# Performance work log

Measured on AMD Instinct MI355X. Metric: run time of the kernel, lower is better.

The kernel has to match this reference:

```python
import jax, jax.numpy as jnp
import numpy as np
from functools import partial

LEAK = 1.0 / 3.0   # scn default leakiness 0.333
EPS = 1e-4         # scn BatchNormalization default eps


def linkey(c, S):
    return (c[..., 0] * S + c[..., 1]) * S + c[..., 2]


def sub_offsets(K):
    r = K // 2
    g = np.stack(np.meshgrid(*([np.arange(-r, r + 1)] * 3), indexing='ij'), -1).reshape(-1, 3)
    return jnp.asarray(g, jnp.int32)


def down_offsets(s):
    g = np.stack(np.meshgrid(*([np.arange(s)] * 3), indexing='ij'), -1).reshape(-1, 3)
    return jnp.asarray(g, jnp.int32)


@partial(jax.checkpoint, static_argnums=(4, 5))
def sparse_conv(out_coords, in_coords, in_feats, W, S_in, stride, offsets):
    """Rulebook gather-GEMM-scatter via sorted-key binary search.
    out_coords [M,3], in_coords [N,3] sorted by linearized key, in_feats [N,Cin],
    W [K3,Cin,Cout]. Submanifold: stride=1, centered offsets, out_coords==in_coords.
    Strided scn.Convolution: offsets 0..stride-1, out sites = unique(in//stride)."""
    in_keys = linkey(in_coords, S_in)  # sorted [N]
    Nin = in_keys.shape[0]

    def body(acc, kw):
        off, Wk = kw
        child = out_coords * stride + off                       # [M,3]
        valid = jnp.all((child >= 0) & (child < S_in), axis=-1)
        nkey = linkey(child, S_in)
        idx = jnp.searchsorted(in_keys, nkey)
        idxc = jnp.clip(idx, 0, Nin - 1)
        found = valid & (in_keys[idxc] == nkey)
        g = jnp.where(found[:, None], in_feats[idxc], 0.0)      # gather, zero for inactive
        return acc + g @ Wk, None

    acc0 = jnp.zeros((out_coords.shape[0], W.shape[-1]), in_feats.dtype)
    acc, _ = jax.lax.scan(body, acc0, (offsets, W))
    return acc


def bn_lrelu(x, g, b):
    m = x.mean(0)
    v = x.var(0)
    y = (x - m) * (g / jnp.sqrt(v + EPS)) + b
    return jnp.where(y > 0, y, LEAK * y)


def lrelu(x):
    return jnp.where(x > 0, x, LEAK * x)


def forward_core(floats, c0, c1, c2, c3, c4):
    (feats0, W_init, Wd1, gd1, bd1, W11a, g11, b11, W11b,
     W12a, g12, b12, W12b, Wd2, gd2, bd2,
     W21a, g21, b21, W21b, W22a, g22, b22, W22b,
     Wd3, gd3, bd3, Wd4, gd4, bd4, W2, b2, W3, b3) = floats
    o3 = sub_offsets(3)
    x = sparse_conv(c0, c0, feats0, W_init, 512, 1, sub_offsets(7))                 # [N0,64] @512
    x = bn_lrelu(sparse_conv(c1, c0, x, Wd1, 512, 2, down_offsets(2)), gd1, bd1)    # [N1,64] @256
    res = x
    h = bn_lrelu(sparse_conv(c1, c1, x, W11a, 256, 1, o3), g11, b11)
    x = lrelu(sparse_conv(c1, c1, h, W11b, 256, 1, o3) + res)
    res = x
    h = bn_lrelu(sparse_conv(c1, c1, x, W12a, 256, 1, o3), g12, b12)
    x = lrelu(sparse_conv(c1, c1, h, W12b, 256, 1, o3) + res)
    x = bn_lrelu(sparse_conv(c2, c1, x, Wd2, 256, 2, down_offsets(2)), gd2, bd2)    # [N2,128] @128
    res = x
    h = bn_lrelu(sparse_conv(c2, c2, x, W21a, 128, 1, o3), g21, b21)
    x = lrelu(sparse_conv(c2, c2, h, W21b, 128, 1, o3) + res)
    res = x
    h = bn_lrelu(sparse_conv(c2, c2, x, W22a, 128, 1, o3), g22, b22)
    x = lrelu(sparse_conv(c2, c2, h, W22b, 128, 1, o3) + res)
    x = bn_lrelu(sparse_conv(c3, c2, x, Wd3, 128, 4, down_offsets(4)), gd3, bd3)    # [N3,64] @32
    x = bn_lrelu(sparse_conv(c4, c3, x, Wd4, 32, 4, down_offsets(4)), gd4, bd4)     # [N4,2]  @8
    # SparseToDense -> dense [2,8,8,8], then torch .view(-1, 2*8*8*8) (channel-major)
    k4 = linkey(c4, 8)
    dense = jnp.zeros((8 * 8 * 8, 2), x.dtype).at[k4].set(x)    # [512,2]
    flat = dense.T.reshape(1, -1)                               # [1,1024]
    v = jax.nn.elu(flat @ W2 + b2)
    return jax.nn.sigmoid(v @ W3 + b3)                          # [1,1]


def _decode(k, S):
    a = k // (S * S)
    r = k % (S * S)
    return np.stack([a, r // S, r % S], -1).astype(np.int32)


def setup_inputs() -> dict:
    rng = np.random.default_rng(0)
    N0 = 50000
    k0 = np.unique(rng.integers(0, 512 ** 3, size=N0 + 20000))[:N0]
    c0 = _decode(k0, 512)
    c1 = _decode(np.unique((c0[:, 0].astype(np.int64) // 2 * 256 + c0[:, 1] // 2) * 256 + c0[:, 2] // 2), 256)
    c2 = _decode(np.unique((c1[:, 0].astype(np.int64) // 2 * 128 + c1[:, 1] // 2) * 128 + c1[:, 2] // 2), 128)
    c3 = _decode(np.unique((c2[:, 0].astype(np.int64) // 4 * 32 + c2[:, 1] // 4) * 32 + c2[:, 2] // 4), 32)
    c4 = _decode(np.unique((c3[:, 0].astype(np.int64) // 4 * 8 + c3[:, 1] // 4) * 8 + c3[:, 2] // 4), 8)
    key = jax.random.key(0)
    ks = jax.random.split(key, 20)

    def w(i, shape, fan):
        return jax.random.normal(ks[i], shape, jnp.float32) / np.float32(np.sqrt(fan))

    return dict(
        feats0=jax.random.normal(ks[0], (N0, 1), jnp.float32),
        W_init=w(1, (343, 1, 64), 343.0),
        Wd1=w(2, (8, 64, 64), 8 * 64), gd1=jnp.ones(64), bd1=jnp.zeros(64),
        W11a=w(3, (27, 64, 64), 27 * 64), g11=jnp.ones(64), b11=jnp.zeros(64),
        W11b=w(4, (27, 64, 64), 27 * 64),
        W12a=w(5, (27, 64, 64), 27 * 64), g12=jnp.ones(64), b12=jnp.zeros(64),
        W12b=w(6, (27, 64, 64), 27 * 64),
        Wd2=w(7, (8, 64, 128), 8 * 64), gd2=jnp.ones(128), bd2=jnp.zeros(128),
        W21a=w(8, (27, 128, 128), 27 * 128), g21=jnp.ones(128), b21=jnp.zeros(128),
        W21b=w(9, (27, 128, 128), 27 * 128),
        W22a=w(10, (27, 128, 128), 27 * 128), g22=jnp.ones(128), b22=jnp.zeros(128),
        W22b=w(11, (27, 128, 128), 27 * 128),
        Wd3=w(12, (64, 128, 64), 64 * 128), gd3=jnp.ones(64), bd3=jnp.zeros(64),
        Wd4=w(13, (64, 64, 2), 64 * 64), gd4=jnp.ones(2), bd4=jnp.zeros(2),
        W2=w(14, (1024, 2), 1024.0), b2=jnp.zeros(2),
        W3=w(15, (2, 1), 2.0), b3=jnp.zeros(1),
        coords0=jnp.asarray(c0), coords1=jnp.asarray(c1), coords2=jnp.asarray(c2),
        coords3=jnp.asarray(c3), coords4=jnp.asarray(c4),
    )


def reference(feats0, W_init, Wd1, gd1, bd1, W11a, g11, b11, W11b, W12a, g12, b12, W12b,
              Wd2, gd2, bd2, W21a, g21, b21, W21b, W22a, g22, b22, W22b,
              Wd3, gd3, bd3, Wd4, gd4, bd4, W2, b2, W3, b3,
              coords0, coords1, coords2, coords3, coords4):
    floats = (feats0, W_init, Wd1, gd1, bd1, W11a, g11, b11, W11b, W12a, g12, b12, W12b,
              Wd2, gd2, bd2, W21a, g21, b21, W21b, W22a, g22, b22, W22b,
              Wd3, gd3, bd3, Wd4, gd4, bd4, W2, b2, W3, b3)
    return forward_core(floats, coords0, coords1, coords2, coords3, coords4)
```

## Files before the change

### kernel.cpp

```cpp
#include <hip/hip_runtime.h>

#define LEAKF (1.0f/3.0f)
#define BN_EPS 1e-4f

__device__ __forceinline__ unsigned hmix(int key) {
    unsigned h = (unsigned)key * 2654435761u;
    h ^= h >> 15;
    return h;
}

__device__ __forceinline__ int hlookup(const int* __restrict__ hk,
                                       const int* __restrict__ hv,
                                       int mask, int key) {
    unsigned h = hmix(key) & (unsigned)mask;
    while (true) {
        int k = hk[h];
        if (k == key) return hv[h];
        if (k == -1) return -1;
        h = (h + 1) & (unsigned)mask;
    }
}

__global__ void build_hash(const int* __restrict__ coords, int N, int S,
                           int* __restrict__ hk, int* __restrict__ hv, int mask) {
    int i = blockIdx.x * blockDim.x + threadIdx.x;
    if (i >= N) return;
    int key = (coords[3 * i] * S + coords[3 * i + 1]) * S + coords[3 * i + 2];
    unsigned h = hmix(key) & (unsigned)mask;
    while (true) {
        int old = atomicCAS(&hk[h], -1, key);
        if (old == -1 || old == key) { hv[h] = i; break; }
        h = (h + 1) & (unsigned)mask;
    }
}

__global__ void build_bitmap(const int* __restrict__ coords, int N,
                             unsigned* __restrict__ bm) {
    int i = blockIdx.x * blockDim.x + threadIdx.x;
    if (i >= N) return;
    int key = (coords[3 * i] * 512 + coords[3 * i + 1]) * 512 + coords[3 * i + 2];
    atomicOr(&bm[key >> 5], 1u << (key & 31));
}

__device__ __forceinline__ float bnl(float v, float s, float h) {
    v = v * s + h;
    return v > 0.f ? v : v * LEAKF;
}

__global__ __launch_bounds__(256) void rb_sub(
    int N, const int* __restrict__ coords,
    const int* __restrict__ hk, const int* __restrict__ hv, int mask,
    int S, int2* __restrict__ pairs, int* __restrict__ counts, int cap) {
    __shared__ int lcnt[27];
    __shared__ int lbase[27];
    int tid = threadIdx.x;
    if (tid < 27) lcnt[tid] = 0;
    __syncthreads();
    int t = blockIdx.x * 256 + tid;
    int k = -1, m = -1, idx = -1, rank = 0;
    if (t < N * 26) {
        m = t / 26;
        int kt = t - m * 26;
        k = kt < 13 ? kt : kt + 1;
        int a = k / 9, b = (k / 3) % 3, c = k % 3;
        int x = coords[3 * m] + a - 1;
        int y = coords[3 * m + 1] + b - 1;
        int z = coords[3 * m + 2] + c - 1;
        if ((unsigned)x < (unsigned)S && (unsigned)y < (unsigned)S &&
            (unsigned)z < (unsigned)S) {
            idx = hlookup(hk, hv, mask, (x * S + y) * S + z);
            if (idx >= 0) rank = atomicAdd(&lcnt[k], 1);
        }
    }
    __syncthreads();
    if (tid < 27 && lcnt[tid] > 0) lbase[tid] = atomicAdd(&counts[tid], lcnt[tid]);
    __syncthreads();
    if (idx >= 0) {
        int p = lbase[k] + rank;
        if (p < cap) pairs[(size_t)k * cap + p] = make_int2(m, idx);
    }
}

__global__ __launch_bounds__(256) void rb_down(
    int Nin, const int* __restrict__ cin,
    const int* __restrict__ hk, const int* __restrict__ hv, int mask,
    int Sout, int s, int2* __restrict__ pairs, int* __restrict__ counts, int cap) {
    __shared__ int lcnt[64];
    __shared__ int lbase[64];
    int tid = threadIdx.x;
    int K3 = s * s * s;
    if (tid < K3) lcnt[tid] = 0;
    __syncthreads();
    int i = blockIdx.x * 256 + tid;
    int k = -1, m = -1, rank = 0;
    if (i < Nin) {
        int x = cin[3 * i], y = cin[3 * i + 1], z = cin[3 * i + 2];
        k = ((x % s) * s + (y % s)) * s + (z % s);
        int key = ((x / s) * Sout + (y / s)) * Sout + (z / s);
        m = hlookup(hk, hv, mask, key);
        rank = atomicAdd(&lcnt[k], 1);
    }
    __syncthreads();
    if (tid < K3 && lcnt[tid] > 0) lbase[tid] = atomicAdd(&counts[tid], lcnt[tid]);
    __syncthreads();
    if (i < Nin) {
        int p = lbase[k] + rank;
        if (p < cap) pairs[(size_t)k * cap + p] = make_int2(m, i);
    }
}

__global__ __launch_bounds__(256) void init_probe(
    int total, const int* __restrict__ c0, const unsigned* __restrict__ bm,
    const int* __restrict__ hk, const int* __restrict__ hv, int mask,
    int2* __restrict__ pairs, int* __restrict__ pcount, int cap) {
    __shared__ int lcnt, lbase;
    int tid = threadIdx.x;
    if (tid == 0) lcnt = 0;
    __syncthreads();
    int t = blockIdx.x * 256 + tid;
    unsigned bits = 0;
    int m = -1, kmin = 0, z = 0, dx = 0, dy = 0, rank = 0;
    if (t < total) {
        m = t / 49;
        int od = t - m * 49;
        dx = od / 7 - 3;
        dy = od - (od / 7) * 7 - 3;
        int x = c0[3 * m] + dx;
        int y = c0[3 * m + 1] + dy;
        z = c0[3 * m + 2];
        if ((unsigned)x < 512u && (unsigned)y < 512u) {
            int zmin = z - 3 < 0 ? 0 : z - 3;
            int zmax = z + 3 > 511 ? 511 : z + 3;
            kmin = (x * 512 + y) * 512 + zmin;
            int wi = kmin >> 5, sh = kmin & 31, nb = zmax - zmin + 1;
            unsigned long long w =
                ((unsigned long long)bm[wi + 1] << 32) | (unsigned long long)bm[wi];
            bits = (unsigned)((w >> sh) & ((1u << nb) - 1u));
            if (dx == 0 && dy == 0) bits &= ~(1u << (z - zmin));
            if (bits) rank = atomicAdd(&lcnt, __popc(bits));
        }
    }
    __syncthreads();
    if (tid == 0 && lcnt > 0) lbase = atomicAdd(pcount, lcnt);
    __syncthreads();
    while (bits) {
        int b = __ffs(bits) - 1;
        bits &= bits - 1;
        int nkey = kmin + b;
        int idx = hlookup(hk, hv, mask, nkey);
        int dz = (kmin & 511) + b - z;
        int k = (dx + 3) * 49 + (dy + 3) * 7 + (dz + 3);
        int p = lbase + rank++;
        if (p < cap) pairs[p] = make_int2(m, idx | (k << 17));
    }
}

__global__ __launch_bounds__(256) void init_center(
    int N0, const float* __restrict__ f0, const float* __restrict__ W,
    float* __restrict__ out) {
    int t = blockIdx.x * 256 + threadIdx.x;
    if (t >= N0 * 64) return;
    int m = t >> 6, co = t & 63;
    out[t] = f0[m] * W[171 * 64 + co];
}

__global__ __launch_bounds__(256) void init_apply(
    const int2* __restrict__ pairs, const int* __restrict__ pcount, int cap,
    const float* __restrict__ f0, const float* __restrict__ W,
    float* __restrict__ out) {
    int P = min(*pcount, cap);
    int t = blockIdx.x * 256 + threadIdx.x;
    if (t >= P * 64) return;
    int p = t >> 6, co = t & 63;
    int2 pr = pairs[p];
    int idx = pr.y & 0x1FFFF, k = pr.y >> 17;
    atomicAdd(&out[(size_t)pr.x * 64 + co], f0[idx] * W[k * 64 + co]);
}

template <int C, int TS, bool BNF>
__global__ __launch_bounds__(256) void center_gemm(
    int N, const float* __restrict__ inF, const float* __restrict__ Wc,
    float* __restrict__ out, const float* __restrict__ scp,
    const float* __restrict__ shp) {
    constexpr int C4 = C / 4;
    constexpr int SP = TS / 8;
    __shared__ float sW[C * 64];
    __shared__ float4 sRow[TS * C4];
    int tid = threadIdx.x;
    int t0 = blockIdx.x * TS;
    int co0 = blockIdx.y << 6;
    for (int e = tid; e < C * 16; e += 256) {
        int ci = e >> 4, c4 = e & 15;
        ((float4*)sW)[e] = *(const float4*)(Wc + (size_t)ci * C + co0 + c4 * 4);
    }
    for (int e = tid; e < TS * C4; e += 256) {
        int p = e / C4, c4 = e - p * C4;
        float4 v = make_float4(0.f, 0.f, 0.f, 0.f);
        if (t0 + p < N) {
            v = ((const float4*)inF)[(size_t)(t0 + p) * C4 + c4];
            if (BNF) {
                float4 s4 = ((const float4*)scp)[c4];
                float4 h4 = ((const float4*)shp)[c4];
                v.x = bnl(v.x, s4.x, h4.x);
                v.y = bnl(v.y, s4.y, h4.y);
                v.z = bnl(v.z, s4.z, h4.z);
                v.w = bnl(v.w, s4.w, h4.w);
            }
        }
        sRow[e] = v;
    }
    __syncthreads();
    int co = tid & 31, sg = tid >> 5;
    float accA[SP], accB[SP];
#pragma unroll
    for (int j = 0; j < SP; j++) { accA[j] = 0.f; accB[j] = 0.f; }
    for (int c4 = 0; c4 < C4; c4++) {
        float a0 = sW[(c4 * 4 + 0) * 64 + co];
        float a1 = sW[(c4 * 4 + 1) * 64 + co];
        float a2 = sW[(c4 * 4 + 2) * 64 + co];
        float a3 = sW[(c4 * 4 + 3) * 64 + co];
        float b0 = sW[(c4 * 4 + 0) * 64 + co + 32];
        float b1 = sW[(c4 * 4 + 1) * 64 + co + 32];
        float b2 = sW[(c4 * 4 + 2) * 64 + co + 32];
        float b3 = sW[(c4 * 4 + 3) * 64 + co + 32];
#pragma unroll
        for (int j = 0; j < SP; j++) {
            float4 r = sRow[(sg * SP + j) * C4 + c4];
            accA[j] += r.x * a0 + r.y * a1 + r.z * a2 + r.w * a3;
            accB[j] += r.x * b0 + r.y * b1 + r.z * b2 + r.w * b3;
        }
    }
#pragma unroll
    for (int j = 0; j < SP; j++) {
        int p = sg * SP + j;
        if (t0 + p < N) {
            out[(size_t)(t0 + p) * C + co0 + co] = accA[j];
            out[(size_t)(t0 + p) * C + co0 + co + 32] = accB[j];
        }
    }
}

template <int CIN, int P, bool BNF>
__global__ __launch_bounds__(256) void pair_gemm(
    const float* __restrict__ inF, const float* __restrict__ W, float* __restrict__ out,
    const int2* __restrict__ pairs, const int* __restrict__ counts,
    int cap, int chunksPerK, int COUT,
    const float* __restrict__ scp, const float* __restrict__ shp) {
    constexpr int C4 = CIN / 4;
    constexpr int SP = P / 8;
    __shared__ float sW[CIN * 64];
    __shared__ float4 sRow[P * C4];
    __shared__ int sM[P];
    __shared__ int sIdx[P];
    int k = blockIdx.x / chunksPerK;
    int chunk = blockIdx.x - k * chunksPerK;
    int cnt = min(counts[k], cap);
    int base = chunk * P;
    if (base >= cnt) return;
    int Pact = min(P, cnt - base);
    int tid = threadIdx.x;
    if (tid < P) {
        if (tid < Pact) {
            int2 pr = pairs[(size_t)k * cap + base + tid];
            sM[tid] = pr.x;
            sIdx[tid] = pr.y;
        } else {
            sM[tid] = -1;
            sIdx[tid] = 0;
        }
    }
    __syncthreads();
    int co0 = blockIdx.y << 6;
    const float* gW = W + (size_t)k * CIN * COUT + co0;
    for (int e = tid; e < CIN * 16; e += 256) {
        int ci = e >> 4, c4 = e & 15;
        ((float4*)sW)[e] = *(const float4*)(gW + (size_t)ci * COUT + c4 * 4);
    }
    for (int e = tid; e < P * C4; e += 256) {
        int p = e / C4, c4 = e - p * C4;
        float4 v = make_float4(0.f, 0.f, 0.f, 0.f);
        if (p < Pact) {
            v = ((const float4*)inF)[(size_t)sIdx[p] * C4 + c4];
            if (BNF) {
                float4 s4 = ((const float4*)scp)[c4];
                float4 h4 = ((const float4*)shp)[c4];
                v.x = bnl(v.x, s4.x, h4.x);
                v.y = bnl(v.y, s4.y, h4.y);
                v.z = bnl(v.z, s4.z, h4.z);
                v.w = bnl(v.w, s4.w, h4.w);
            }
        }
        sRow[e] = v;
    }
    __syncthreads();
    int co = tid & 31, sg = tid >> 5;
    float accA[SP], accB[SP];
#pragma unroll
    for (int j = 0; j < SP; j++) { accA[j] = 0.f; accB[j] = 0.f; }
    for (int c4 = 0; c4 < C4; c4++) {
        float a0 = sW[(c4 * 4 + 0) * 64 + co];
        float a1 = sW[(c4 * 4 + 1) * 64 + co];
        float a2 = sW[(c4 * 4 + 2) * 64 + co];
        float a3 = sW[(c4 * 4 + 3) * 64 + co];
        float b0 = sW[(c4 * 4 + 0) * 64 + co + 32];
        float b1 = sW[(c4 * 4 + 1) * 64 + co + 32];
        float b2 = sW[(c4 * 4 + 2) * 64 + co + 32];
        float b3 = sW[(c4 * 4 + 3) * 64 + co + 32];
#pragma unroll
        for (int j = 0; j < SP; j++) {
            float4 r = sRow[(sg * SP + j) * C4 + c4];
            accA[j] += r.x * a0 + r.y * a1 + r.z * a2 + r.w * a3;
            accB[j] += r.x * b0 + r.y * b1 + r.z * b2 + r.w * b3;
        }
    }
#pragma unroll
    for (int j = 0; j < SP; j++) {
        int p = sg * SP + j;
        if (p < Pact) {
            atomicAdd(&out[(size_t)sM[p] * COUT + co0 + co], accA[j]);
            atomicAdd(&out[(size_t)sM[p] * COUT + co0 + co + 32], accB[j]);
        }
    }
}

__global__ __launch_bounds__(64) void convd4_kernel(
    int M, const int* __restrict__ oc, const float* __restrict__ x3,
    const float* __restrict__ W, float* __restrict__ out4,
    const int* __restrict__ hk, const int* __restrict__ hv, int mask,
    const float* __restrict__ scp, const float* __restrict__ shp) {
    __shared__ int sIdx[64];
    __shared__ int sK[64];
    __shared__ int sCount;
    int m = blockIdx.x, tid = threadIdx.x;
    int cx = oc[3 * m], cy = oc[3 * m + 1], cz = oc[3 * m + 2];
    if (tid == 0) sCount = 0;
    __syncthreads();
    {
        int k = tid;
        int a = k >> 4, b = (k >> 2) & 3, c = k & 3;
        int x = cx * 4 + a, y = cy * 4 + b, z = cz * 4 + c;
        int key = (x * 32 + y) * 32 + z;
        int idx = hlookup(hk, hv, mask, key);
        if (idx >= 0) { int p = atomicAdd(&sCount, 1); sIdx[p] = idx; sK[p] = k; }
    }
    __syncthreads();
    int cnt = sCount;
    float s = scp[tid], h = shp[tid];
    float a0 = 0.f, a1 = 0.f;
    for (int j = 0; j < cnt; j++) {
        int idx = sIdx[j], k = sK[j];
        float f = bnl(x3[(size_t)idx * 64 + tid], s, h);
        const float* wk = W + ((size_t)k * 64 + tid) * 2;
        a0 += f * wk[0];
        a1 += f * wk[1];
    }
    for (int o = 32; o > 0; o >>= 1) {
        a0 += __shfl_down(a0, o);
        a1 += __shfl_down(a1, o);
    }
    if (tid == 0) { out4[2 * m] = a0; out4[2 * m + 1] = a1; }
}

__global__ __launch_bounds__(256) void bn_reduce_fin(
    const float4* __restrict__ X4, int total4, int B4, int C, int Cmask, float invN,
    const float* __restrict__ g, const float* __restrict__ b,
    float* __restrict__ sums, int* __restrict__ done,
    float* __restrict__ sc, float* __restrict__ sh) {
    __shared__ float sS[128];
    __shared__ float sQ[128];
    __shared__ int isLast;
    int tid = threadIdx.x;
    if (tid < C) { sS[tid] = 0.f; sQ[tid] = 0.f; }
    __syncthreads();
    int base4 = blockIdx.x * B4;
    int end4 = min(base4 + B4, total4);
    float s0 = 0.f, s1 = 0.f, s2 = 0.f, s3 = 0.f;
    float q0 = 0.f, q1 = 0.f, q2 = 0.f, q3 = 0.f;
    for (int e4 = base4 + tid; e4 < end4; e4 += 256) {
        float4 v = X4[e4];
        s0 += v.x; q0 += v.x * v.x;
        s1 += v.y; q1 += v.y * v.y;
        s2 += v.z; q2 += v.z * v.z;
        s3 += v.w; q3 += v.w * v.w;
    }
    int c0 = (4 * (base4 + tid)) & Cmask;
    atomicAdd(&sS[c0], s0);           atomicAdd(&sQ[c0], q0);
    atomicAdd(&sS[(c0 + 1) & Cmask], s1); atomicAdd(&sQ[(c0 + 1) & Cmask], q1);
    atomicAdd(&sS[(c0 + 2) & Cmask], s2); atomicAdd(&sQ[(c0 + 2) & Cmask], q2);
    atomicAdd(&sS[(c0 + 3) & Cmask], s3); atomicAdd(&sQ[(c0 + 3) & Cmask], q3);
    __syncthreads();
    if (tid < C) {
        atomicAdd(&sums[tid], sS[tid]);
        atomicAdd(&sums[128 + tid], sQ[tid]);
    }
    __syncthreads();
    if (tid == 0) {
        __threadfence();
        int t = atomicAdd(done, 1);
        isLast = (t == (int)gridDim.x - 1);
    }
    __syncthreads();
    if (isLast) {
        if (tid < C) {
            float v1 = atomicAdd(&sums[tid], 0.0f);
            float v2 = atomicAdd(&sums[128 + tid], 0.0f);
            float mean = v1 * invN;
            float var = v2 * invN - mean * mean;
            float s = g[tid] / sqrtf(var + BN_EPS);
            sc[tid] = s;
            sh[tid] = b[tid] - mean * s;
            sums[tid] = 0.f;
            sums[128 + tid] = 0.f;
        }
        if (tid == 0) *done = 0;
    }
}

__global__ __launch_bounds__(256) void add_lrelu(const float4* __restrict__ A,
                                                 const float4* __restrict__ R,
                                                 float4* __restrict__ Y, int total4) {
    int e = blockIdx.x * 256 + threadIdx.x;
    if (e >= total4) return;
    float4 a = A[e], r = R[e], v;
    v.x = a.x + r.x; v.y = a.y + r.y; v.z = a.z + r.z; v.w = a.w + r.w;
    v.x = v.x > 0.f ? v.x : v.x * LEAKF;
    v.y = v.y > 0.f ? v.y : v.y * LEAKF;
    v.z = v.z > 0.f ? v.z : v.z * LEAKF;
    v.w = v.w > 0.f ? v.w : v.w * LEAKF;
    Y[e] = v;
}

__global__ __launch_bounds__(256) void add_lrelu_bn(const float4* __restrict__ A,
                                                    const float4* __restrict__ X,
                                                    float4* __restrict__ Y, int total4,
                                                    int C4mask,
                                                    const float* __restrict__ scp,
                                                    const float* __restrict__ shp) {
    int e = blockIdx.x * 256 + threadIdx.x;
    if (e >= total4) return;
    int c4 = e & C4mask;
    float4 s4 = ((const float4*)scp)[c4];
    float4 h4 = ((const float4*)shp)[c4];
    float4 a = A[e], x = X[e], v;
    v.x = a.x + bnl(x.x, s4.x, h4.x);
    v.y = a.y + bnl(x.y, s4.y, h4.y);
    v.z = a.z + bnl(x.z, s4.z, h4.z);
    v.w = a.w + bnl(x.w, s4.w, h4.w);
    v.x = v.x > 0.f ? v.x : v.x * LEAKF;
    v.y = v.y > 0.f ? v.y : v.y * LEAKF;
    v.z = v.z > 0.f ? v.z : v.z * LEAKF;
    v.w = v.w > 0.f ? v.w : v.w * LEAKF;
    Y[e] = v;
}

__global__ __launch_bounds__(256) void bn_scatter(int M, const int* __restrict__ c4,
                                                  const float* __restrict__ x4,
                                                  const float* __restrict__ sc,
                                                  const float* __restrict__ sh,
                                                  float* __restrict__ dense) {
    int i = blockIdx.x * 256 + threadIdx.x;
    if (i >= 2 * M) return;
    int m = i >> 1, co = i & 1;
    float v = x4[i] * sc[co] + sh[co];
    v = v > 0.f ? v : v * LEAKF;
    int key = (c4[3 * m] * 8 + c4[3 * m + 1]) * 8 + c4[3 * m + 2];
    dense[key * 2 + co] = v;
}

__global__ __launch_bounds__(256) void head_kernel(const float* __restrict__ dense,
                                                   const float* __restrict__ W2,
                                                   const float* __restrict__ b2,
                                                   const float* __restrict__ W3,
                                                   const float* __restrict__ b3,
                                                   float* __restrict__ out) {
    __shared__ float r0[256];
    __shared__ float r1[256];
    int tid = threadIdx.x;
    float a0 = 0.f, a1 = 0.f;
    for (int j = tid; j < 1024; j += 256) {
        int co = j >> 9, k = j & 511;
        float f = dense[k * 2 + co];
        a0 += f * W2[2 * j];
        a1 += f * W2[2 * j + 1];
    }
    r0[tid] = a0;
    r1[tid] = a1;
    __syncthreads();
    for (int s = 128; s > 0; s >>= 1) {
        if (tid < s) { r0[tid] += r0[tid + s]; r1[tid] += r1[tid + s]; }
        __syncthreads();
    }
    if (tid == 0) {
        float v0 = r0[0] + b2[0];
        float v1 = r1[0] + b2[1];
        v0 = v0 > 0.f ? v0 : expm1f(v0);
        v1 = v1 > 0.f ? v1 : expm1f(v1);
        float z = v0 * W3[0] + v1 * W3[1] + b3[0];
        out[0] = 1.f / (1.f + expf(-z));
    }
}

extern "C" void kernel_launch(void* const* d_in, const int* in_sizes, int n_in,
                              void* d_out, int out_size, void* d_ws, size_t ws_size,
                              hipStream_t stream) {
    const float* F0    = (const float*)d_in[0];
    const float* Winit = (const float*)d_in[1];
    const float* Wd1   = (const float*)d_in[2];
    const float* gd1   = (const float*)d_in[3];
    const float* bd1   = (const float*)d_in[4];
    const float* W11a  = (const float*)d_in[5];
    const float* g11   = (const float*)d_in[6];
    const float* b11   = (const float*)d_in[7];
    const float* W11b  = (const float*)d_in[8];
    const float* W12a  = (const float*)d_in[9];
    const float* g12   = (const float*)d_in[10];
    const float* b12   = (const float*)d_in[11];
    const float* W12b  = (const float*)d_in[12];
    const float* Wd2   = (const float*)d_in[13];
    const float* gd2   = (const float*)d_in[14];
    const float* bd2   = (const float*)d_in[15];
    const float* W21a  = (const float*)d_in[16];
    const float* g21   = (const float*)d_in[17];
    const float* b21   = (const float*)d_in[18];
    const float* W21b  = (const float*)d_in[19];
    const float* W22a  = (const float*)d_in[20];
    const float* g22   = (const float*)d_in[21];
    const float* b22   = (const float*)d_in[22];
    const float* W22b  = (const float*)d_in[23];
    const float* Wd3   = (const float*)d_in[24];
    const float* gd3   = (const float*)d_in[25];
    const float* bd3   = (const float*)d_in[26];
    const float* Wd4   = (const float*)d_in[27];
    const float* gd4   = (const float*)d_in[28];
    const float* bd4   = (const float*)d_in[29];
    const float* W2    = (const float*)d_in[30];
    const float* b2    = (const float*)d_in[31];
    const float* W3    = (const float*)d_in[32];
    const float* b3    = (const float*)d_in[33];
    const int* c0 = (const int*)d_in[34];
    const int* c1 = (const int*)d_in[35];
    const int* c2 = (const int*)d_in[36];
    const int* c3 = (const int*)d_in[37];
    const int* c4 = (const int*)d_in[38];
    int N0 = in_sizes[34] / 3, N1 = in_sizes[35] / 3, N2 = in_sizes[36] / 3;
    int N3 = in_sizes[37] / 3, N4 = in_sizes[38] / 3;

    char* base = (char*)d_ws;
    size_t off = 0;
    auto alloc = [&](size_t bytes) -> void* {
        void* p = base + off;
        off = (off + bytes + 255) & ~(size_t)255;
        return p;
    };
    const int CAP0 = 262144, CAP = 131072, CAP3 = 65536;
    size_t hs_off = off;
    int* hk0 = (int*)alloc((size_t)CAP0 * 4);
    int* hv0 = (int*)alloc((size_t)CAP0 * 4);
    int* hk1 = (int*)alloc((size_t)CAP * 4);
    int* hv1 = (int*)alloc((size_t)CAP * 4);
    int* hk2 = (int*)alloc((size_t)CAP * 4);
    int* hv2 = (int*)alloc((size_t)CAP * 4);
    int* hk3 = (int*)alloc((size_t)CAP3 * 4);
    int* hv3 = (int*)alloc((size_t)CAP3 * 4);
    size_t he_off = off;
    size_t zs_off = off;
    float* sums = (float*)alloc(256 * 4);
    float* scb = (float*)alloc(8 * 128 * 4);
    float* shb = (float*)alloc(8 * 128 * 4);
    float* dense = (float*)alloc(1024 * 4);
    float* x4 = (float*)alloc(1032 * 4);
    int* counts = (int*)alloc(136 * 4);
    size_t ze_off = off;
    int* cntS1 = counts, *cntS2 = counts + 27, *cntD1 = counts + 54, *cntD2 = counts + 62,
       * cntD3 = counts + 70;
    int* done = counts + 134;
    int* pcount = counts + 135;
    const int CAP_S1 = 1024, CAP_S2 = 4096, CAP_D1 = 8192, CAP_D2 = 8192, CAP_D3 = 1024;
    const int CAPP = 16384;
    int2* pairs0 = (int2*)alloc((size_t)CAPP * 8);
    int2* rbS1 = (int2*)alloc((size_t)27 * CAP_S1 * 8);
    int2* rbS2 = (int2*)alloc((size_t)27 * CAP_S2 * 8);
    int2* rbD1 = (int2*)alloc((size_t)8 * CAP_D1 * 8);
    int2* rbD2 = (int2*)alloc((size_t)8 * CAP_D2 * 8);
    int2* rbD3 = (int2*)alloc((size_t)64 * CAP_D3 * 8);
    size_t relems = (size_t)N0 * 64;
    if ((size_t)N2 * 128 > relems) relems = (size_t)N2 * 128;
    float* R1 = (float*)alloc(relems * 4);
    float* R2 = (float*)alloc(relems * 4);
    float* R3 = (float*)alloc(relems * 4);
    unsigned* bitmap = (unsigned*)R1;

    hipMemsetAsync(base + hs_off, 0xFF, he_off - hs_off, stream);
    hipMemsetAsync(base + zs_off, 0x00, ze_off - zs_off, stream);
    hipMemsetAsync(bitmap, 0x00, (size_t)(1 << 24) + 64, stream);

    build_hash<<<(N0 + 255) / 256, 256, 0, stream>>>(c0, N0, 512, hk0, hv0, CAP0 - 1);
    build_hash<<<(N1 + 255) / 256, 256, 0, stream>>>(c1, N1, 256, hk1, hv1, CAP - 1);
    build_hash<<<(N2 + 255) / 256, 256, 0, stream>>>(c2, N2, 128, hk2, hv2, CAP - 1);
    build_hash<<<(N3 + 255) / 256, 256, 0, stream>>>(c3, N3, 32, hk3, hv3, CAP3 - 1);
    build_bitmap<<<(N0 + 255) / 256, 256, 0, stream>>>(c0, N0, bitmap);
    rb_sub<<<(N1 * 26 + 255) / 256, 256, 0, stream>>>(N1, c1, hk1, hv1, CAP - 1, 256,
                                                      rbS1, cntS1, CAP_S1);
    rb_sub<<<(N2 * 26 + 255) / 256, 256, 0, stream>>>(N2, c2, hk2, hv2, CAP - 1, 128,
                                                      rbS2, cntS2, CAP_S2);
    rb_down<<<(N0 + 255) / 256, 256, 0, stream>>>(N0, c0, hk1, hv1, CAP - 1, 256, 2,
                                                  rbD1, cntD1, CAP_D1);
    rb_down<<<(N1 + 255) / 256, 256, 0, stream>>>(N1, c1, hk2, hv2, CAP - 1, 128, 2,
                                                  rbD2, cntD2, CAP_D2);
    rb_down<<<(N2 + 255) / 256, 256, 0, stream>>>(N2, c2, hk3, hv3, CAP3 - 1, 32, 4,
                                                  rbD3, cntD3, CAP_D3);

    auto bnstats = [&](const float* X, int N, int C, const float* g, const float* b,
                       int slot) {
        int total4 = (N * C + 3) >> 2;
        int B4 = 32 * C;
        int grid = (total4 + B4 - 1) / B4;
        bn_reduce_fin<<<grid, 256, 0, stream>>>((const float4*)X, total4, B4, C, C - 1,
                                                1.0f / (float)N, g, b, sums, done,
                                                scb + slot * 128, shb + slot * 128);
    };
    auto sub64 = [&](const float* X, const float* W, float* Y, int slot) {
        if (slot >= 0) {
            center_gemm<64, 64, true><<<dim3((N1 + 63) / 64, 1), 256, 0, stream>>>(
                N1, X, W + 13 * 64 * 64, Y, scb + slot * 128, shb + slot * 128);
            pair_gemm<64, 64, true><<<dim3(27 * (CAP_S1 / 64), 1), 256, 0, stream>>>(
                X, W, Y, rbS1, cntS1, CAP_S1, CAP_S1 / 64, 64,
                scb + slot * 128, shb + slot * 128);
        } else {
            center_gemm<64, 64, false><<<dim3((N1 + 63) / 64, 1), 256, 0, stream>>>(
                N1, X, W + 13 * 64 * 64, Y, nullptr, nullptr);
            pair_gemm<64, 64, false><<<dim3(27 * (CAP_S1 / 64), 1), 256, 0, stream>>>(
                X, W, Y, rbS1, cntS1, CAP_S1, CAP_S1 / 64, 64, nullptr, nullptr);
        }
    };
    auto sub128 = [&](const float* X, const float* W, float* Y, int slot) {
        const int CH2 = (CAP_S2 + 47) / 48;
        if (slot >= 0) {
            center_gemm<128, 48, true><<<dim3((N2 + 47) / 48, 2), 256, 0, stream>>>(
                N2, X, W + 13 * 128 * 128, Y, scb + slot * 128, shb + slot * 128);
            pair_gemm<128, 48, true><<<dim3(27 * CH2, 2), 256, 0, stream>>>(
                X, W, Y, rbS2, cntS2, CAP_S2, CH2, 128, scb + slot * 128, shb + slot * 128);
        } else {
            center_gemm<128, 48, false><<<dim3((N2 + 47) / 48, 2), 256, 0, stream>>>(
                N2, X, W + 13 * 128 * 128, Y, nullptr, nullptr);
            pair_gemm<128, 48, false><<<dim3(27 * CH2, 2), 256, 0, stream>>>(
                X, W, Y, rbS2, cntS2, CAP_S2, CH2, 128, nullptr, nullptr);
        }
    };

    int totProbe = N0 * 49;
    init_probe<<<(totProbe + 255) / 256, 256, 0, stream>>>(totProbe, c0, bitmap,
                                                           hk0, hv0, CAP0 - 1,
                                                           pairs0, pcount, CAPP);
    init_center<<<(N0 * 64 + 255) / 256, 256, 0, stream>>>(N0, F0, Winit, R3);
    init_apply<<<(CAPP * 64) / 256, 256, 0, stream>>>(pairs0, pcount, CAPP, F0, Winit, R3);

    hipMemsetAsync(R1, 0, (size_t)N1 * 64 * 4, stream);
    pair_gemm<64, 64, false><<<dim3(8 * (CAP_D1 / 64), 1), 256, 0, stream>>>(
        R3, Wd1, R1, rbD1, cntD1, CAP_D1, CAP_D1 / 64, 64, nullptr, nullptr);
    bnstats(R1, N1, 64, gd1, bd1, 0);

    sub64(R1, W11a, R2, 0);
    bnstats(R2, N1, 64, g11, b11, 1);
    sub64(R2, W11b, R3, 1);
    add_lrelu_bn<<<(N1 * 16 + 255) / 256, 256, 0, stream>>>(
        (const float4*)R3, (const float4*)R1, (float4*)R2, N1 * 16, 15, scb, shb);
    sub64(R2, W12a, R3, -1);
    bnstats(R3, N1, 64, g12, b12, 2);
    sub64(R3, W12b, R1, 2);
    add_lrelu<<<(N1 * 16 + 255) / 256, 256, 0, stream>>>(
        (const float4*)R1, (const float4*)R2, (float4*)R2, N1 * 16);

    hipMemsetAsync(R1, 0, (size_t)N2 * 128 * 4, stream);
    pair_gemm<64, 64, false><<<dim3(8 * (CAP_D2 / 64), 2), 256, 0, stream>>>(
        R2, Wd2, R1, rbD2, cntD2, CAP_D2, CAP_D2 / 64, 128, nullptr, nullptr);
    bnstats(R1, N2, 128, gd2, bd2, 3);

    sub128(R1, W21a, R2, 3);
    bnstats(R2, N2, 128, g21, b21, 4);
    sub128(R2, W21b, R3, 4);
    add_lrelu_bn<<<(N2 * 32 + 255) / 256, 256, 0, stream>>>(
        (const float4*)R3, (const float4*)R1, (float4*)R2, N2 * 32, 31,
        scb + 3 * 128, shb + 3 * 128);
    sub128(R2, W22a, R3, -1);
    bnstats(R3, N2, 128, g22, b22, 5);
    sub128(R3, W22b, R1, 5);
    add_lrelu<<<(N2 * 32 + 255) / 256, 256, 0, stream>>>(
        (const float4*)R1, (const float4*)R2, (float4*)R3, N2 * 32);

    hipMemsetAsync(R1, 0, (size_t)N3 * 64 * 4, stream);
    {
        const int CH3 = (CAP_D3 + 47) / 48;
        pair_gemm<128, 48, false><<<dim3(64 * CH3, 1), 256, 0, stream>>>(
            R3, Wd3, R1, rbD3, cntD3, CAP_D3, CH3, 64, nullptr, nullptr);
    }
    bnstats(R1, N3, 64, gd3, bd3, 6);

    convd4_kernel<<<N4, 64, 0, stream>>>(N4, c4, R1, Wd4, x4, hk3, hv3, CAP3 - 1,
                                         scb + 6 * 128, shb + 6 * 128);
    bnstats(x4, N4, 2, gd4, bd4, 7);
    bn_scatter<<<(2 * N4 + 255) / 256, 256, 0, stream>>>(N4, c4, x4, scb + 7 * 128,
                                                         shb + 7 * 128, dense);

    head_kernel<<<1, 256, 0, stream>>>(dense, W2, b2, W3, b3, (float*)d_out);
}
```

Baseline: 1.199 ms.

## Merge hash/bitmap builds and rulebook kernels; use occupancy bitmaps for submanifold probes

Four build_hash launches plus the bitmap build become one launch, and the three rb_down launches become one, each block choosing its level by block index. This cuts launch count and per-launch overhead. Submanifold rulebook construction now builds occupancy bitmaps for levels 1 and 2. It scans the three z-neighbours of each (dx,dy) column with a single 64-bit bitmap read and probes the hash only for occupied sites, using 9 threads per site instead of 26. The cost is larger zeroed bitmap buffers and more divergent per-thread loops.

Result: faster. 1.123 ms (-6.3%).

```diff
diff --git a/kernel.cpp b/kernel.cpp
--- a/kernel.cpp
+++ b/kernel.cpp
@@ -21,11 +21,30 @@
     }
 }
 
-__global__ void build_hash(const int* __restrict__ coords, int N, int S,
-                           int* __restrict__ hk, int* __restrict__ hv, int mask) {
-    int i = blockIdx.x * blockDim.x + threadIdx.x;
+__device__ __forceinline__ float bnl(float v, float s, float h) {
+    v = v * s + h;
+    return v > 0.f ? v : v * LEAKF;
+}
+
+__global__ __launch_bounds__(256) void build_hash_bm_all(
+    int B0, int B1, int B2,
+    int N0, const int* __restrict__ c0, int* __restrict__ hk0, int* __restrict__ hv0,
+    int m0, unsigned* __restrict__ bm0,
+    int N1, const int* __restrict__ c1, int* __restrict__ hk1, int* __restrict__ hv1,
+    int m1, unsigned* __restrict__ bm1,
+    int N2, const int* __restrict__ c2, int* __restrict__ hk2, int* __restrict__ hv2,
+    int m2, unsigned* __restrict__ bm2,
+    int N3, const int* __restrict__ c3, int* __restrict__ hk3, int* __restrict__ hv3,
+    int m3) {
+    const int* coords; int* hk; int* hv; unsigned* bm; int mask, S, N, i;
+    int b = blockIdx.x;
+    if (b < B0)           { coords = c0; hk = hk0; hv = hv0; bm = bm0; mask = m0; S = 512; N = N0; i = b * 256 + threadIdx.x; }
+    else if (b < B0 + B1) { coords = c1; hk = hk1; hv = hv1; bm = bm1; mask = m1; S = 256; N = N1; i = (b - B0) * 256 + threadIdx.x; }
+    else if (b < B0 + B1 + B2) { coords = c2; hk = hk2; hv = hv2; bm = bm2; mask = m2; S = 128; N = N2; i = (b - B0 - B1) * 256 + threadIdx.x; }
+    else                  { coords = c3; hk = hk3; hv = hv3; bm = nullptr; mask = m3; S = 32; N = N3; i = (b - B0 - B1 - B2) * 256 + threadIdx.x; }
     if (i >= N) return;
     int key = (coords[3 * i] * S + coords[3 * i + 1]) * S + coords[3 * i + 2];
+    if (bm) atomicOr(&bm[key >> 5], 1u << (key & 31));
     unsigned h = hmix(key) & (unsigned)mask;
     while (true) {
         int old = atomicCAS(&hk[h], -1, key);
@@ -34,64 +53,109 @@
     }
 }
 
-__global__ void build_bitmap(const int* __restrict__ coords, int N,
-                             unsigned* __restrict__ bm) {
-    int i = blockIdx.x * blockDim.x + threadIdx.x;
-    if (i >= N) return;
-    int key = (coords[3 * i] * 512 + coords[3 * i + 1]) * 512 + coords[3 * i + 2];
-    atomicOr(&bm[key >> 5], 1u << (key & 31));
-}
-
-__device__ __forceinline__ float bnl(float v, float s, float h) {
-    v = v * s + h;
-    return v > 0.f ? v : v * LEAKF;
-}
-
-__global__ __launch_bounds__(256) void rb_sub(
-    int N, const int* __restrict__ coords,
-    const int* __restrict__ hk, const int* __restrict__ hv, int mask,
-    int S, int2* __restrict__ pairs, int* __restrict__ counts, int cap) {
+__global__ __launch_bounds__(256) void rb_sub_bm(
+    int B1,
+    int N1, const int* __restrict__ c1, const unsigned* __restrict__ bm1,
+    const int* __restrict__ hk1, const int* __restrict__ hv1, int m1,
+    int2* __restrict__ rb1, int* __restrict__ cnt1, int cap1,
+    int N2, const int* __restrict__ c2, const unsigned* __restrict__ bm2,
+    const int* __restrict__ hk2, const int* __restrict__ hv2, int m2,
+    int2* __restrict__ rb2, int* __restrict__ cnt2, int cap2) {
     __shared__ int lcnt[27];
     __shared__ int lbase[27];
     int tid = threadIdx.x;
     if (tid < 27) lcnt[tid] = 0;
     __syncthreads();
-    int t = blockIdx.x * 256 + tid;
-    int k = -1, m = -1, idx = -1, rank = 0;
-    if (t < N * 26) {
-        m = t / 26;
-        int kt = t - m * 26;
-        k = kt < 13 ? kt : kt + 1;
-        int a = k / 9, b = (k / 3) % 3, c = k % 3;
-        int x = coords[3 * m] + a - 1;
-        int y = coords[3 * m + 1] + b - 1;
-        int z = coords[3 * m + 2] + c - 1;
-        if ((unsigned)x < (unsigned)S && (unsigned)y < (unsigned)S &&
-            (unsigned)z < (unsigned)S) {
-            idx = hlookup(hk, hv, mask, (x * S + y) * S + z);
-            if (idx >= 0) rank = atomicAdd(&lcnt[k], 1);
+    const int* coords; const unsigned* bm; const int* hk; const int* hv;
+    int mask, S, N, t; int2* pairs; int* counts; int cap;
+    if (blockIdx.x < B1) {
+        coords = c1; bm = bm1; hk = hk1; hv = hv1; mask = m1; S = 256; N = N1;
+        pairs = rb1; counts = cnt1; cap = cap1; t = blockIdx.x * 256 + tid;
+    } else {
+        coords = c2; bm = bm2; hk = hk2; hv = hv2; mask = m2; S = 128; N = N2;
+        pairs = rb2; counts = cnt2; cap = cap2; t = (blockIdx.x - B1) * 256 + tid;
+    }
+    unsigned bits = 0;
+    int m = 0, kmin = 0, z = 0, dx = 0, dy = 0;
+    int rk[3], ix[3];
+    if (t < N * 9) {
+        m = t / 9;
+        int od = t - m * 9;
+        dx = od / 3 - 1;
+        dy = od - (od / 3) * 3 - 1;
+        int x = coords[3 * m] + dx;
+        int y = coords[3 * m + 1] + dy;
+        z = coords[3 * m + 2];
+        if ((unsigned)x < (unsigned)S && (unsigned)y < (unsigned)S) {
+            int zmin = z - 1 < 0 ? 0 : z - 1;
+            int zmax = z + 1 > S - 1 ? S - 1 : z + 1;
+            kmin = (x * S + y) * S + zmin;
+            int wi = kmin >> 5, sh = kmin & 31, nb = zmax - zmin + 1;
+            unsigned long long w =
+                ((unsigned long long)bm[wi + 1] << 32) | (unsigned long long)bm[wi];
+            bits = (unsigned)((w >> sh) & ((1u << nb) - 1u));
+            if (dx == 0 && dy == 0) bits &= ~(1u << (z - zmin));
+            unsigned tmp = bits;
+            int nf = 0;
+            while (tmp) {
+                int bb = __ffs(tmp) - 1;
+                tmp &= tmp - 1;
+                ix[nf] = hlookup(hk, hv, mask, kmin + bb);
+                int dz = (kmin & (S - 1)) + bb - z;
+                int k = (dx + 1) * 9 + (dy + 1) * 3 + (dz + 1);
+                rk[nf] = atomicAdd(&lcnt[k], 1);
+                nf++;
+            }
         }
     }
     __syncthreads();
     if (tid < 27 && lcnt[tid] > 0) lbase[tid] = atomicAdd(&counts[tid], lcnt[tid]);
     __syncthreads();
-    if (idx >= 0) {
-        int p = lbase[k] + rank;
-        if (p < cap) pairs[(size_t)k * cap + p] = make_int2(m, idx);
-    }
-}
-
-__global__ __launch_bounds__(256) void rb_down(
-    int Nin, const int* __restrict__ cin,
-    const int* __restrict__ hk, const int* __restrict__ hv, int mask,
-    int Sout, int s, int2* __restrict__ pairs, int* __restrict__ counts, int cap) {
+    {
+        unsigned tmp = bits;
+        int j = 0;
+        while (tmp) {
+            int bb = __ffs(tmp) - 1;
+            tmp &= tmp - 1;
+            int dz = (kmin & (S - 1)) + bb - z;
+            int k = (dx + 1) * 9 + (dy + 1) * 3 + (dz + 1);
+            int p = lbase[k] + rk[j];
+            if (p < cap) pairs[(size_t)k * cap + p] = make_int2(m, ix[j]);
+            j++;
+        }
+    }
+}
+
+__global__ __launch_bounds__(256) void rb_down_all(
+    int B1, int B2,
+    int N0, const int* __restrict__ c0, const int* __restrict__ hk1,
+    const int* __restrict__ hv1, int m1, int2* __restrict__ rbD1,
+    int* __restrict__ cntD1, int capD1,
+    int N1, const int* __restrict__ c1, const int* __restrict__ hk2,
+    const int* __restrict__ hv2, int m2, int2* __restrict__ rbD2,
+    int* __restrict__ cntD2, int capD2,
+    int N2, const int* __restrict__ c2, const int* __restrict__ hk3,
+    const int* __restrict__ hv3, int m3, int2* __restrict__ rbD3,
+    int* __restrict__ cntD3, int capD3) {
     __shared__ int lcnt[64];
     __shared__ int lbase[64];
     int tid = threadIdx.x;
+    const int* cin; const int* hk; const int* hv;
+    int mask, Sout, s, Nin, i; int2* pairs; int* counts; int cap;
+    int b = blockIdx.x;
+    if (b < B1) {
+        cin = c0; hk = hk1; hv = hv1; mask = m1; Sout = 256; s = 2; Nin = N0;
+        pairs = rbD1; counts = cntD1; cap = capD1; i = b * 256 + tid;
+    } else if (b < B1 + B2) {
+        cin = c1; hk = hk2; hv = hv2; mask = m2; Sout = 128; s = 2; Nin = N1;
+        pairs = rbD2; counts = cntD2; cap = capD2; i = (b - B1) * 256 + tid;
+    } else {
+        cin = c2; hk = hk3; hv = hv3; mask = m3; Sout = 32; s = 4; Nin = N2;
+        pairs = rbD3; counts = cntD3; cap = capD3; i = (b - B1 - B2) * 256 + tid;
+    }
     int K3 = s * s * s;
     if (tid < K3) lcnt[tid] = 0;
     __syncthreads();
-    int i = blockIdx.x * 256 + tid;
     int k = -1, m = -1, rank = 0;
     if (i < Nin) {
         int x = cin[3 * i], y = cin[3 * i + 1], z = cin[3 * i + 2];
@@ -384,7 +448,7 @@
         s3 += v.w; q3 += v.w * v.w;
     }
     int c0 = (4 * (base4 + tid)) & Cmask;
-    atomicAdd(&sS[c0], s0);           atomicAdd(&sQ[c0], q0);
+    atomicAdd(&sS[c0], s0);               atomicAdd(&sQ[c0], q0);
     atomicAdd(&sS[(c0 + 1) & Cmask], s1); atomicAdd(&sQ[(c0 + 1) & Cmask], q1);
     atomicAdd(&sS[(c0 + 2) & Cmask], s2); atomicAdd(&sQ[(c0 + 2) & Cmask], q2);
     atomicAdd(&sS[(c0 + 3) & Cmask], s3); atomicAdd(&sQ[(c0 + 3) & Cmask], q3);
@@ -570,6 +634,8 @@
     float* dense = (float*)alloc(1024 * 4);
     float* x4 = (float*)alloc(1032 * 4);
     int* counts = (int*)alloc(136 * 4);
+    unsigned* bm1 = (unsigned*)alloc((size_t)(524288 + 2) * 4);
+    unsigned* bm2 = (unsigned*)alloc((size_t)(65536 + 2) * 4);
     size_t ze_off = off;
     int* cntS1 = counts, *cntS2 = counts + 27, *cntD1 = counts + 54, *cntD2 = counts + 62,
        * cntD3 = counts + 70;
@@ -588,27 +654,30 @@
     float* R1 = (float*)alloc(relems * 4);
     float* R2 = (float*)alloc(relems * 4);
     float* R3 = (float*)alloc(relems * 4);
-    unsigned* bitmap = (unsigned*)R1;
+    unsigned* bm0 = (unsigned*)R1;
 
     hipMemsetAsync(base + hs_off, 0xFF, he_off - hs_off, stream);
     hipMemsetAsync(base + zs_off, 0x00, ze_off - zs_off, stream);
-    hipMemsetAsync(bitmap, 0x00, (size_t)(1 << 24) + 64, stream);
-
-    build_hash<<<(N0 + 255) / 256, 256, 0, stream>>>(c0, N0, 512, hk0, hv0, CAP0 - 1);
-    build_hash<<<(N1 + 255) / 256, 256, 0, stream>>>(c1, N1, 256, hk1, hv1, CAP - 1);
-    build_hash<<<(N2 + 255) / 256, 256, 0, stream>>>(c2, N2, 128, hk2, hv2, CAP - 1);
-    build_hash<<<(N3 + 255) / 256, 256, 0, stream>>>(c3, N3, 32, hk3, hv3, CAP3 - 1);
-    build_bitmap<<<(N0 + 255) / 256, 256, 0, stream>>>(c0, N0, bitmap);
-    rb_sub<<<(N1 * 26 + 255) / 256, 256, 0, stream>>>(N1, c1, hk1, hv1, CAP - 1, 256,
-                                                      rbS1, cntS1, CAP_S1);
-    rb_sub<<<(N2 * 26 + 255) / 256, 256, 0, stream>>>(N2, c2, hk2, hv2, CAP - 1, 128,
-                                                      rbS2, cntS2, CAP_S2);
-    rb_down<<<(N0 + 255) / 256, 256, 0, stream>>>(N0, c0, hk1, hv1, CAP - 1, 256, 2,
-                                                  rbD1, cntD1, CAP_D1);
-    rb_down<<<(N1 + 255) / 256, 256, 0, stream>>>(N1, c1, hk2, hv2, CAP - 1, 128, 2,
-                                                  rbD2, cntD2, CAP_D2);
-    rb_down<<<(N2 + 255) / 256, 256, 0, stream>>>(N2, c2, hk3, hv3, CAP3 - 1, 32, 4,
-                                                  rbD3, cntD3, CAP_D3);
+    hipMemsetAsync(bm0, 0x00, (size_t)(1 << 24) + 64, stream);
+
+    int Bh0 = (N0 + 255) / 256, Bh1 = (N1 + 255) / 256, Bh2 = (N2 + 255) / 256,
+        Bh3 = (N3 + 255) / 256;
+    build_hash_bm_all<<<Bh0 + Bh1 + Bh2 + Bh3, 256, 0, stream>>>(
+        Bh0, Bh1, Bh2,
+        N0, c0, hk0, hv0, CAP0 - 1, bm0,
+        N1, c1, hk1, hv1, CAP - 1, bm1,
+        N2, c2, hk2, hv2, CAP - 1, bm2,
+        N3, c3, hk3, hv3, CAP3 - 1);
+    int Bs1 = (N1 * 9 + 255) / 256, Bs2 = (N2 * 9 + 255) / 256;
+    rb_sub_bm<<<Bs1 + Bs2, 256, 0, stream>>>(
+        Bs1,
+        N1, c1, bm1, hk1, hv1, CAP - 1, rbS1, cntS1, CAP_S1,
+        N2, c2, bm2, hk2, hv2, CAP - 1, rbS2, cntS2, CAP_S2);
+    rb_down_all<<<Bh0 + Bh1 + Bh2, 256, 0, stream>>>(
+        Bh0, Bh1,
+        N0, c0, hk1, hv1, CAP - 1, rbD1, cntD1, CAP_D1,
+        N1, c1, hk2, hv2, CAP - 1, rbD2, cntD2, CAP_D2,
+        N2, c2, hk3, hv3, CAP3 - 1, rbD3, cntD3, CAP_D3);
 
     auto bnstats = [&](const float* X, int N, int C, const float* g, const float* b,
                        int slot) {
@@ -649,7 +718,7 @@
     };
 
     int totProbe = N0 * 49;
-    init_probe<<<(totProbe + 255) / 256, 256, 0, stream>>>(totProbe, c0, bitmap,
+    init_probe<<<(totProbe + 255) / 256, 256, 0, stream>>>(totProbe, c0, bm0,
                                                            hk0, hv0, CAP0 - 1,
                                                            pairs0, pcount, CAPP);
     init_center<<<(N0 * 64 + 255) / 256, 256, 0, stream>>>(N0, F0, Winit, R3);
```
